# Performance work log

Measured on AMD Instinct MI355X. Metric: run time of the kernel, lower is better.

The kernel has to match this reference:

```python
import jax, jax.numpy as jnp
import numpy as np

N = 50000      # nodes
E = 800000     # edges
IN = 128       # in_dim
OUT = 128      # out_dim
R = 4          # num_relations
H = 8          # heads
D = OUT // H   # per-head dim
NEG_SLOPE = 0.2


def setup_inputs() -> dict:
    key = jax.random.key(0)
    ks = jax.random.split(key, 12)
    s = 0.05
    return {
        "node_inp": jax.random.normal(ks[0], (N, IN), dtype=jnp.float32),
        "edge_index": jax.random.randint(ks[1], (2, E), 0, N),
        "edge_type": jax.random.randint(ks[2], (E,), 0, R),
        # per-relation GATConv params
        "W_rel": jax.random.normal(ks[3], (R, IN, OUT), dtype=jnp.float32) * s,
        "att_src_rel": jax.random.normal(ks[4], (R, H, D), dtype=jnp.float32) * s,
        "att_dst_rel": jax.random.normal(ks[5], (R, H, D), dtype=jnp.float32) * s,
        "bias_rel": jax.random.normal(ks[6], (R, OUT), dtype=jnp.float32) * s,
        # linear layers
        "W_self": jax.random.normal(ks[7], (IN, OUT), dtype=jnp.float32) * s,   # lin_self
        "W_cross": jax.random.normal(ks[8], (OUT, OUT), dtype=jnp.float32) * s,  # lin_cross
        # lang_conv GAT params (lin_l is Bypass, so no weight matrix)
        "att_src_lang": jax.random.normal(ks[9], (H, D), dtype=jnp.float32) * s,
        "att_dst_lang": jax.random.normal(ks[10], (H, D), dtype=jnp.float32) * s,
        "bias_lang": jax.random.normal(ks[11], (OUT,), dtype=jnp.float32) * s,
    }


def _hgnn_forward(node_inp, edge_index, edge_type, W_rel, att_src_rel,
                  att_dst_rel, bias_rel, W_self, W_cross,
                  att_src_lang, att_dst_lang, bias_lang):
    src, dst = edge_index[0], edge_index[1]

    def rel_gat(W, a_s, a_d, b, mask):
        # standard PyG GATConv (single x, add_self_loops=False), restricted to
        # edges with this relation type via mask
        x = (node_inp @ W).reshape(N, H, D)                     # [N,H,D]
        es = jnp.einsum('nhd,hd->nh', x, a_s)
        ed = jnp.einsum('nhd,hd->nh', x, a_d)
        logit = jax.nn.leaky_relu(es[src] + ed[dst], NEG_SLOPE)  # [E,H]
        logit = jnp.where(mask[:, None], logit, -1e30)
        mx = jax.ops.segment_max(logit, dst, num_segments=N)     # [N,H]
        mx = jnp.maximum(mx, -1e30)                              # avoid -inf
        p = jnp.exp(logit - mx[dst]) * mask[:, None]
        den = jax.ops.segment_sum(p, dst, num_segments=N)        # [N,H]
        alpha = p / jnp.where(den > 0, den, 1.0)[dst]            # [E,H]
        msg = alpha[..., None] * x[src]                          # [E,H,D]
        out = jax.ops.segment_sum(msg, dst, num_segments=N)      # [N,H,D]
        tmask = jax.ops.segment_sum(mask.astype(jnp.float32), dst,
                                    num_segments=N) > 0          # [N] target nodes
        return out.reshape(N, OUT) + b, tmask

    rel_masks = edge_type[None, :] == jnp.arange(R)[:, None]     # [R,E]
    rel_out, tmask = jax.vmap(rel_gat)(W_rel, att_src_rel, att_dst_rel,
                                       bias_rel, rel_masks)      # [R,N,OUT],[R,N]
    h = jax.nn.gelu(rel_out, approximate=False) @ W_cross        # [R,N,OUT]

    S = node_inp @ W_self                                        # [N,OUT] self entries
    # lang_conv: per node i, GAT attention over entries {self(i)} U
    # {rel outputs at i for relations where i is a target}. lin_l = Bypass,
    # and since x is a single tensor in PyG, x_dst = rel_inputs[i] = S[i].
    ent = jnp.concatenate([S[None], h], axis=0).reshape(R + 1, N, H, D)
    valid = jnp.concatenate([jnp.ones((1, N), bool), tmask], axis=0)  # [R+1,N]
    ls = jnp.einsum('knhd,hd->knh', ent, att_src_lang)
    ld = jnp.einsum('nhd,hd->nh', ent[0], att_dst_lang)
    logit = jax.nn.leaky_relu(ls + ld[None], NEG_SLOPE)          # [R+1,N,H]
    logit = jnp.where(valid[..., None], logit, -jnp.inf)
    alpha = jax.nn.softmax(logit, axis=0)                        # self always valid
    out = jnp.einsum('knh,knhd->nhd', alpha, ent).reshape(N, OUT)
    return out + bias_lang


def reference(node_inp, edge_index, edge_type, W_rel, att_src_rel, att_dst_rel,
              bias_rel, W_self, W_cross, att_src_lang, att_dst_lang, bias_lang):
    return _hgnn_forward(node_inp, edge_index, edge_type, W_rel, att_src_rel,
                         att_dst_rel, bias_rel, W_self, W_cross,
                         att_src_lang, att_dst_lang, bias_lang)
```

## Files before the change

### kernel.cpp

```cpp
#include <hip/hip_runtime.h>
#include <hip/hip_bf16.h>
#include <math.h>

#define NN 50000
#define NE 800000
#define NREL 4
#define NHEAD 8
#define NSEG (NREL * NN)
#define BCAP 26

typedef __hip_bfloat16 bf16;
typedef short short8 __attribute__((ext_vector_type(8)));
typedef float floatx4 __attribute__((ext_vector_type(4)));

#define LOG2E 1.4426950408889634f

__device__ __forceinline__ float b2f(bf16 v) { return __bfloat162float(v); }
__device__ __forceinline__ float us2f(unsigned short u) {
    return __uint_as_float(((unsigned)u) << 16);
}
__device__ __forceinline__ unsigned short f2us(float v) {
    bf16 b = __float2bfloat16(v);
    return *(unsigned short*)&b;
}

__device__ __forceinline__ float gelu_f(float v) {
    float z = v * 0.70710678118654752f;
    float az = fabsf(z);
    float t = __builtin_amdgcn_rcpf(__builtin_fmaf(0.3275911f, az, 1.f));
    float p = t * (0.254829592f +
              t * (-0.284496736f +
              t * (1.421413741f +
              t * (-1.453152027f +
              t * 1.061405429f))));
    float ex = __builtin_amdgcn_exp2f(az * az * -LOG2E);
    float er = copysignf(1.f - p * ex, z);
    return 0.5f * v * (1.f + er);
}

__global__ void fill_kernel(float* __restrict__ out, int n) {
    int t = blockIdx.x * blockDim.x + threadIdx.x;
    if (t < n) out[t] = 1000.0f;
}

__global__ void prep_kernel(const float* __restrict__ W_rel,
                            const float* __restrict__ W_self,
                            const float* __restrict__ W_cross,
                            const float* __restrict__ a_src,
                            const float* __restrict__ a_dst,
                            bf16* __restrict__ Wt, bf16* __restrict__ Wct,
                            int* __restrict__ counts) {
    int t = blockIdx.x * blockDim.x + threadIdx.x;
    if (t < NSEG) counts[t] = 0;
    if (t < 768 * 128) {
        int row = t >> 7, k = t & 127;
        float v;
        if (row < 512) {
            int r = row >> 7, c = row & 127;
            v = W_rel[(r * 128 + k) * 128 + c];
        } else if (row < 640) {
            v = W_self[k * 128 + (row - 512)];
        } else if (row < 704) {
            int q = row - 640;
            bool is_src = q < 32;
            int qq = is_src ? q : q - 32;
            int r = qq >> 3, h = qq & 7;
            const float* av = (is_src ? a_src : a_dst) + (r * 8 + h) * 16;
            const float* wr = W_rel + (size_t)(r * 128 + k) * 128 + h * 16;
            float s = 0.f;
            #pragma unroll
            for (int dd = 0; dd < 16; ++dd) s += wr[dd] * av[dd];
            v = s * LOG2E;
        } else {
            v = 0.f;
        }
        Wt[t] = __float2bfloat16(v);
    } else if (t < 768 * 128 + 128 * 128) {
        int u = t - 768 * 128;
        int n = u >> 7, k = u & 127;
        Wct[u] = __float2bfloat16(W_cross[k * 128 + n]);
    }
}

__global__ __launch_bounds__(256) void gemm_node(
    const float* __restrict__ Ain,
    const bf16* __restrict__ Bt,
    bf16* __restrict__ outb,
    float* __restrict__ outf,
    unsigned short* __restrict__ es_u,
    unsigned short* __restrict__ ed_u,
    const int* __restrict__ ei,
    const int* __restrict__ et,
    int* __restrict__ counts,
    unsigned short* __restrict__ bkt,
    int M)
{
    if (blockIdx.y == 0) {
        int idx = blockIdx.x * 256 + threadIdx.x;
        int stride = gridDim.x * 256;
        for (int e = idx; e < NE; e += stride) {
            int seg = et[e] * NN + ei[NE + e];
            int pos = atomicAdd(&counts[seg], 1);
            if (pos < BCAP) bkt[(unsigned)seg * BCAP + pos] = (unsigned short)ei[e];
        }
        return;
    }

    __shared__ __align__(16) char smem[17408];
    short (*As)[40] = (short (*)[40])smem;
    short (*Bs)[40] = (short (*)[40])(smem + 5120);

    const int tid  = threadIdx.x;
    const int wave = tid >> 6, lane = tid & 63;
    const int quad = lane >> 4, l16 = lane & 15;
    const int wr_ = wave & 1, wc = wave >> 1;
    const int row0 = blockIdx.x * 64;
    const int col0 = (blockIdx.y - 1) * 128;

    floatx4 acc[2][4];
    #pragma unroll
    for (int i = 0; i < 2; ++i)
        #pragma unroll
        for (int j = 0; j < 4; ++j) acc[i][j] = (floatx4){0.f, 0.f, 0.f, 0.f};

    for (int k0 = 0; k0 < 128; k0 += 32) {
        {
            int c = tid;
            int r = c >> 2, off = (c & 3) * 8;
            int gr = row0 + r;
            short8 v = {0, 0, 0, 0, 0, 0, 0, 0};
            if (gr < M) {
                const float* ap = Ain + (((size_t)gr) << 7) + k0 + off;
                float4 f0 = *(const float4*)ap;
                float4 f1 = *(const float4*)(ap + 4);
                v = (short8){(short)f2us(f0.x), (short)f2us(f0.y),
                             (short)f2us(f0.z), (short)f2us(f0.w),
                             (short)f2us(f1.x), (short)f2us(f1.y),
                             (short)f2us(f1.z), (short)f2us(f1.w)};
            }
            *(short8*)&As[r][off] = v;
        }
        #pragma unroll
        for (int i = 0; i < 2; ++i) {
            int c = tid * 2 + i;
            int r = c >> 2, off = (c & 3) * 8;
            short8 w = *(const short8*)(Bt + (((size_t)(col0 + r)) << 7) + k0 + off);
            *(short8*)&Bs[r][off] = w;
        }
        __syncthreads();

        short8 av[2], bv[4];
        #pragma unroll
        for (int mt = 0; mt < 2; ++mt)
            av[mt] = *(const short8*)&As[wr_ * 32 + mt * 16 + l16][quad * 8];
        #pragma unroll
        for (int nt = 0; nt < 4; ++nt)
            bv[nt] = *(const short8*)&Bs[wc * 64 + nt * 16 + l16][quad * 8];
        #pragma unroll
        for (int mt = 0; mt < 2; ++mt)
            #pragma unroll
            for (int nt = 0; nt < 4; ++nt)
                acc[mt][nt] = __builtin_amdgcn_mfma_f32_16x16x32_bf16(
                    av[mt], bv[nt], acc[mt][nt], 0, 0, 0);
        __syncthreads();
    }

    if (blockIdx.y == 6) {
        if (wc == 0) {
            #pragma unroll
            for (int mt = 0; mt < 2; ++mt) {
                #pragma unroll
                for (int reg = 0; reg < 4; ++reg) {
                    int gr = row0 + wr_ * 32 + mt * 16 + quad * 4 + reg;
                    if (gr >= M) continue;
                    #pragma unroll
                    for (int nt = 0; nt < 4; ++nt) {
                        int q = nt * 16 + l16;
                        unsigned short v = f2us(acc[mt][nt][reg]);
                        if (q < 32)
                            es_u[(unsigned)((q >> 3) * NN + gr) * 8u + (unsigned)(q & 7)] = v;
                        else
                            ed_u[(unsigned)(((q - 32) >> 3) * NN + gr) * 8u + (unsigned)((q - 32) & 7)] = v;
                    }
                }
            }
        }
        return;
    }

    float* ct = (float*)(smem + wave * 4352);
    const int rr2 = lane >> 2;
    const int cc0 = (lane & 3) * 16;

    for (int mt = 0; mt < 2; ++mt) {
        #pragma unroll
        for (int nt = 0; nt < 4; ++nt)
            #pragma unroll
            for (int reg = 0; reg < 4; ++reg)
                ct[(quad * 4 + reg) * 68 + nt * 16 + l16] = acc[mt][nt][reg];
        __syncthreads();

        int gr2 = row0 + wr_ * 32 + mt * 16 + rr2;
        if (gr2 < M) {
            float4 f0 = *(const float4*)&ct[rr2 * 68 + cc0];
            float4 f1 = *(const float4*)&ct[rr2 * 68 + cc0 + 4];
            float4 f2 = *(const float4*)&ct[rr2 * 68 + cc0 + 8];
            float4 f3 = *(const float4*)&ct[rr2 * 68 + cc0 + 12];
            int cb = wc * 64 + cc0;
            if (blockIdx.y == 5) {
                float* dst = outf + (((size_t)gr2) << 7) + cb;
                ((float4*)dst)[0] = f0;
                ((float4*)dst)[1] = f1;
                ((float4*)dst)[2] = f2;
                ((float4*)dst)[3] = f3;
            } else {
                float tmp[16] = {f0.x, f0.y, f0.z, f0.w, f1.x, f1.y, f1.z, f1.w,
                                 f2.x, f2.y, f2.z, f2.w, f3.x, f3.y, f3.z, f3.w};
                short8 o0, o1;
                #pragma unroll
                for (int j = 0; j < 8; ++j) o0[j] = (short)f2us(tmp[j]);
                #pragma unroll
                for (int j = 0; j < 8; ++j) o1[j] = (short)f2us(tmp[8 + j]);
                bf16* dst = outb + ((size_t)((blockIdx.y - 1) * NN + gr2) << 7) + cb;
                *(short8*)dst = o0;
                *(short8*)(dst + 8) = o1;
            }
        }
        __syncthreads();
    }
}

__global__ __launch_bounds__(256) void agg_kernel(
    const unsigned short* __restrict__ bkt, const int* __restrict__ counts,
    const bf16* __restrict__ Xb, const unsigned short* __restrict__ es_u,
    const unsigned short* __restrict__ ed_u, const float* __restrict__ bias_rel,
    bf16* __restrict__ Gb4, unsigned char* __restrict__ flag)
{
    const int rel = blockIdx.y;
    const int n = blockIdx.x * 4 + (threadIdx.x >> 6);
    if (n >= NN) return;
    const int l = threadIdx.x & 63;
    const int h = l >> 3;
    const int f = l * 2;
    const unsigned seg = (unsigned)(rel * NN + n);
    int cnt = __builtin_amdgcn_readfirstlane(counts[seg]);
    cnt = cnt < BCAP ? cnt : BCAP;
    const unsigned short* bk = bkt + seg * (unsigned)BCAP;
    const float edv = us2f(ed_u[seg * 8u + (unsigned)h]);
    float a0 = 0.f, a1 = 0.f, den = 0.f;
    const unsigned short* Xr = (const unsigned short*)Xb + (unsigned)rel * (unsigned)(NN * 128);
    const unsigned short* esr = es_u + (unsigned)rel * (unsigned)(NN * 8);

    int e = 0;
    for (; e + 3 < cnt; e += 4) {
        int s0 = __builtin_amdgcn_readfirstlane((int)bk[e]);
        int s1 = __builtin_amdgcn_readfirstlane((int)bk[e + 1]);
        int s2 = __builtin_amdgcn_readfirstlane((int)bk[e + 2]);
        int s3 = __builtin_amdgcn_readfirstlane((int)bk[e + 3]);
        float e0 = us2f(esr[(unsigned)s0 * 8u + (unsigned)h]);
        float e1 = us2f(esr[(unsigned)s1 * 8u + (unsigned)h]);
        float e2 = us2f(esr[(unsigned)s2 * 8u + (unsigned)h]);
        float e3 = us2f(esr[(unsigned)s3 * 8u + (unsigned)h]);
        ushort2 u0 = *(const ushort2*)(Xr + (unsigned)s0 * 128u + (unsigned)f);
        ushort2 u1 = *(const ushort2*)(Xr + (unsigned)s1 * 128u + (unsigned)f);
        ushort2 u2 = *(const ushort2*)(Xr + (unsigned)s2 * 128u + (unsigned)f);
        ushort2 u3 = *(const ushort2*)(Xr + (unsigned)s3 * 128u + (unsigned)f);
        float aa0 = e0 + edv, aa1 = e1 + edv, aa2 = e2 + edv, aa3 = e3 + edv;
        float w0 = __builtin_amdgcn_exp2f(fmaxf(aa0, 0.2f * aa0));
        float w1 = __builtin_amdgcn_exp2f(fmaxf(aa1, 0.2f * aa1));
        float w2 = __builtin_amdgcn_exp2f(fmaxf(aa2, 0.2f * aa2));
        float w3 = __builtin_amdgcn_exp2f(fmaxf(aa3, 0.2f * aa3));
        a0 += w0 * us2f(u0.x) + w1 * us2f(u1.x) + w2 * us2f(u2.x) + w3 * us2f(u3.x);
        a1 += w0 * us2f(u0.y) + w1 * us2f(u1.y) + w2 * us2f(u2.y) + w3 * us2f(u3.y);
        den += (w0 + w1) + (w2 + w3);
    }
    for (; e < cnt; ++e) {
        int s0 = __builtin_amdgcn_readfirstlane((int)bk[e]);
        float e0 = us2f(esr[(unsigned)s0 * 8u + (unsigned)h]);
        ushort2 u0 = *(const ushort2*)(Xr + (unsigned)s0 * 128u + (unsigned)f);
        float aa0 = e0 + edv;
        float w0 = __builtin_amdgcn_exp2f(fmaxf(aa0, 0.2f * aa0));
        a0 += w0 * us2f(u0.x);
        a1 += w0 * us2f(u0.y);
        den += w0;
    }

    float inv = den > 0.f ? __builtin_amdgcn_rcpf(den) : 0.f;
    float2 bv = *(const float2*)(bias_rel + (unsigned)rel * 128u + (unsigned)f);
    float v0 = gelu_f(__builtin_fmaf(a0, inv, bv.x));
    float v1 = gelu_f(__builtin_fmaf(a1, inv, bv.y));
    ushort2 o;
    o.x = f2us(v0);
    o.y = f2us(v1);
    *(ushort2*)((unsigned short*)Gb4 + ((unsigned)n * 4u + (unsigned)rel) * 128u + (unsigned)f) = o;
    if (l == 0) flag[(unsigned)n * 4u + (unsigned)rel] = (unsigned char)(cnt > 0);
}

__global__ __launch_bounds__(256) void gemm_lang(
    const bf16* __restrict__ A,
    const bf16* __restrict__ Bt,
    const unsigned char* __restrict__ flag,
    const float* __restrict__ asl_g,
    const float* __restrict__ adl_g,
    const float* __restrict__ bias_lang,
    float* __restrict__ out)
{
    __shared__ __align__(16) char smem[15360];
    short (*As)[40] = (short (*)[40])smem;
    short (*Bs)[40] = (short (*)[40])(smem + 5120);

    const int M = NN * NREL;
    const int tid  = threadIdx.x;
    const int wave = tid >> 6, lane = tid & 63;
    const int quad = lane >> 4, l16 = lane & 15;
    const int wr_ = wave & 1, wc = wave >> 1;
    const int row0 = blockIdx.x * 64;

    floatx4 acc[2][4];
    #pragma unroll
    for (int i = 0; i < 2; ++i)
        #pragma unroll
        for (int j = 0; j < 4; ++j) acc[i][j] = (floatx4){0.f, 0.f, 0.f, 0.f};

    for (int k0 = 0; k0 < 128; k0 += 32) {
        {
            int c = tid;
            int r = c >> 2, off = (c & 3) * 8;
            int gr = row0 + r;
            short8 v = {0, 0, 0, 0, 0, 0, 0, 0};
            if (gr < M)
                v = *(const short8*)(A + (((size_t)gr) << 7) + k0 + off);
            *(short8*)&As[r][off] = v;
        }
        #pragma unroll
        for (int i = 0; i < 2; ++i) {
            int c = tid * 2 + i;
            int r = c >> 2, off = (c & 3) * 8;
            short8 w = *(const short8*)(Bt + (((size_t)r) << 7) + k0 + off);
            *(short8*)&Bs[r][off] = w;
        }
        __syncthreads();

        short8 av[2], bv[4];
        #pragma unroll
        for (int mt = 0; mt < 2; ++mt)
            av[mt] = *(const short8*)&As[wr_ * 32 + mt * 16 + l16][quad * 8];
        #pragma unroll
        for (int nt = 0; nt < 4; ++nt)
            bv[nt] = *(const short8*)&Bs[wc * 64 + nt * 16 + l16][quad * 8];
        #pragma unroll
        for (int mt = 0; mt < 2; ++mt)
            #pragma unroll
            for (int nt = 0; nt < 4; ++nt)
                acc[mt][nt] = __builtin_amdgcn_mfma_f32_16x16x32_bf16(
                    av[mt], bv[nt], acc[mt][nt], 0, 0, 0);
        __syncthreads();
    }

    const int nb0 = blockIdx.x * 16 + wr_ * 8;
    #pragma unroll
    for (int nt = 0; nt < 4; ++nt) {
        int col = wc * 64 + nt * 16 + l16;
        float asl = asl_g[col];
        float adl = adl_g[col];
        float bl  = bias_lang[col];
        #pragma unroll
        for (int mt = 0; mt < 2; ++mt) {
            int node = nb0 + mt * 4 + quad;
            bool ok = node < NN;
            float Sv = ok ? out[(unsigned)node * 128u + (unsigned)col] : 0.f;
            float h0 = acc[mt][nt][0], h1 = acc[mt][nt][1];
            float h2 = acc[mt][nt][2], h3 = acc[mt][nt][3];
            float t0 = h0 * asl, t1 = h1 * asl, t2 = h2 * asl, t3 = h3 * asl;
            float ts = Sv * asl, td = Sv * adl;
            #pragma unroll
            for (int off = 1; off < 16; off <<= 1) {
                t0 += __shfl_xor(t0, off);
                t1 += __shfl_xor(t1, off);
                t2 += __shfl_xor(t2, off);
                t3 += __shfl_xor(t3, off);
                ts += __shfl_xor(ts, off);
                td += __shfl_xor(td, off);
            }
            unsigned fl = ok ? *(const unsigned*)(flag + (unsigned)node * 4u) : 0u;
            float aS = ts + td, a0 = t0 + td, a1 = t1 + td, a2 = t2 + td, a3 = t3 + td;
            float lS = fmaxf(aS, 0.2f * aS);
            float l0 = fmaxf(a0, 0.2f * a0);
            float l1 = fmaxf(a1, 0.2f * a1);
            float l2 = fmaxf(a2, 0.2f * a2);
            float l3 = fmaxf(a3, 0.2f * a3);
            bool v0 = (fl & 0x000000FFu) != 0, v1 = (fl & 0x0000FF00u) != 0;
            bool v2 = (fl & 0x00FF0000u) != 0, v3 = (fl & 0xFF000000u) != 0;
            float m = lS;
            if (v0) m = fmaxf(m, l0);
            if (v1) m = fmaxf(m, l1);
            if (v2) m = fmaxf(m, l2);
            if (v3) m = fmaxf(m, l3);
            float eS = __expf(lS - m);
            float e0 = v0 ? __expf(l0 - m) : 0.f;
            float e1 = v1 ? __expf(l1 - m) : 0.f;
            float e2 = v2 ? __expf(l2 - m) : 0.f;
            float e3 = v3 ? __expf(l3 - m) : 0.f;
            float sum = eS + e0 + e1 + e2 + e3;
            float o = eS * Sv + e0 * h0 + e1 * h1 + e2 * h2 + e3 * h3;
            o = o / sum + bl;
            if (ok) out[(unsigned)node * 128u + (unsigned)col] = o;
        }
    }
}

extern "C" void kernel_launch(void* const* d_in, const int* in_sizes, int n_in,
                              void* d_out, int out_size, void* d_ws, size_t ws_size,
                              hipStream_t stream) {
    const float* node_inp     = (const float*)d_in[0];
    const int*   edge_index   = (const int*)d_in[1];
    const int*   edge_type    = (const int*)d_in[2];
    const float* W_rel        = (const float*)d_in[3];
    const float* att_src_rel  = (const float*)d_in[4];
    const float* att_dst_rel  = (const float*)d_in[5];
    const float* bias_rel     = (const float*)d_in[6];
    const float* W_self       = (const float*)d_in[7];
    const float* W_cross      = (const float*)d_in[8];
    const float* att_src_lang = (const float*)d_in[9];
    const float* att_dst_lang = (const float*)d_in[10];
    const float* bias_lang    = (const float*)d_in[11];
    (void)in_sizes; (void)n_in;

    const size_t SZ_XB   = (size_t)NREL * NN * 128 * 2;
    const size_t SZ_ES   = (size_t)NREL * NN * 8 * 2;
    const size_t SZ_GB4  = (size_t)NREL * NN * 128 * 2;
    const size_t SZ_WT   = 768 * 128 * 2;
    const size_t SZ_WCT  = 128 * 128 * 2;
    const size_t SZ_BKT  = (size_t)NSEG * BCAP * 2;
    const size_t SZ_CNT  = (size_t)NSEG * 4;
    const size_t SZ_FLG  = (size_t)NN * 4;
    const size_t TOTAL = SZ_XB + 2 * SZ_ES + SZ_GB4 + SZ_WT + SZ_WCT +
                         SZ_BKT + SZ_CNT + SZ_FLG;

    if (ws_size < TOTAL) {
        fill_kernel<<<(out_size + 255) / 256, 256, 0, stream>>>((float*)d_out, out_size);
        return;
    }

    char* ws = (char*)d_ws;
    size_t o = 0;
    bf16*  Xb      = (bf16*)(ws + o);  o += SZ_XB;
    unsigned short* es_u = (unsigned short*)(ws + o); o += SZ_ES;
    unsigned short* ed_u = (unsigned short*)(ws + o); o += SZ_ES;
    bf16*  Gb4     = (bf16*)(ws + o);  o += SZ_GB4;
    bf16*  Wt      = (bf16*)(ws + o);  o += SZ_WT;
    bf16*  Wct     = (bf16*)(ws + o);  o += SZ_WCT;
    unsigned short* bkt = (unsigned short*)(ws + o); o += SZ_BKT;
    int*   counts  = (int*)(ws + o);   o += SZ_CNT;
    unsigned char* flag = (unsigned char*)(ws + o);
    float* S       = (float*)d_out;

    prep_kernel<<<(NSEG + 255) / 256, 256, 0, stream>>>(
        W_rel, W_self, W_cross, att_src_rel, att_dst_rel, Wt, Wct, counts);

    dim3 g1((NN + 63) / 64, 7);
    gemm_node<<<g1, 256, 0, stream>>>(node_inp, Wt, Xb, S, es_u, ed_u,
                                      edge_index, edge_type, counts, bkt, NN);

    dim3 ga((NN + 3) / 4, NREL);
    agg_kernel<<<ga, 256, 0, stream>>>(bkt, counts, Xb, es_u, ed_u, bias_rel, Gb4, flag);

    dim3 g2((NREL * NN + 63) / 64, 1);
    gemm_lang<<<g2, 256, 0, stream>>>(Gb4, Wct, flag, att_src_lang, att_dst_lang,
                                      bias_lang, (float*)d_out);
}
```

Before: 297.4 us.

## Load A tile once per block and loop over all six column tiles

The node GEMM previously launched one block per 128-column output tile, so each of the six column tiles re-read and re-converted the fp32 input rows. Now each block converts its 64-row A tile to bf16 once, holds it in registers, and loops over the six column tiles, reading B fragments directly from global memory and dropping the B shared-memory staging. Per-wave block syncs in the epilogue are replaced by a waitcnt because each wave uses a private staging area. The grid shrinks from 7 to 2 in y, which cuts parallelism and serializes more work per block, and there is more register pressure from the held A fragments.

```diff
diff --git a/kernel.cpp b/kernel.cpp
--- a/kernel.cpp
+++ b/kernel.cpp
@@ -106,127 +106,127 @@
         return;
     }
 
-    __shared__ __align__(16) char smem[17408];
-    short (*As)[40] = (short (*)[40])smem;
-    short (*Bs)[40] = (short (*)[40])(smem + 5120);
+    __shared__ __align__(16) char smem[20480];
+    short (*As)[64][40] = (short (*)[64][40])smem;
 
     const int tid  = threadIdx.x;
     const int wave = tid >> 6, lane = tid & 63;
     const int quad = lane >> 4, l16 = lane & 15;
     const int wr_ = wave & 1, wc = wave >> 1;
     const int row0 = blockIdx.x * 64;
-    const int col0 = (blockIdx.y - 1) * 128;
-
-    floatx4 acc[2][4];
-    #pragma unroll
-    for (int i = 0; i < 2; ++i)
-        #pragma unroll
-        for (int j = 0; j < 4; ++j) acc[i][j] = (floatx4){0.f, 0.f, 0.f, 0.f};
-
-    for (int k0 = 0; k0 < 128; k0 += 32) {
-        {
-            int c = tid;
-            int r = c >> 2, off = (c & 3) * 8;
-            int gr = row0 + r;
+
+    {
+        int r = tid >> 2, kc = tid & 3;
+        int gr = row0 + r;
+        const float* ap = Ain + (((size_t)gr) << 7) + kc * 32;
+        #pragma unroll
+        for (int i = 0; i < 4; ++i) {
             short8 v = {0, 0, 0, 0, 0, 0, 0, 0};
             if (gr < M) {
-                const float* ap = Ain + (((size_t)gr) << 7) + k0 + off;
-                float4 f0 = *(const float4*)ap;
-                float4 f1 = *(const float4*)(ap + 4);
+                float4 f0 = *(const float4*)(ap + i * 8);
+                float4 f1 = *(const float4*)(ap + i * 8 + 4);
                 v = (short8){(short)f2us(f0.x), (short)f2us(f0.y),
                              (short)f2us(f0.z), (short)f2us(f0.w),
                              (short)f2us(f1.x), (short)f2us(f1.y),
                              (short)f2us(f1.z), (short)f2us(f1.w)};
             }
-            *(short8*)&As[r][off] = v;
-        }
-        #pragma unroll
-        for (int i = 0; i < 2; ++i) {
-            int c = tid * 2 + i;
-            int r = c >> 2, off = (c & 3) * 8;
-            short8 w = *(const short8*)(Bt + (((size_t)(col0 + r)) << 7) + k0 + off);
-            *(short8*)&Bs[r][off] = w;
-        }
-        __syncthreads();
-
-        short8 av[2], bv[4];
+            *(short8*)&As[kc][r][i * 8] = v;
+        }
+    }
+    __syncthreads();
+
+    short8 av[4][2];
+    #pragma unroll
+    for (int kc = 0; kc < 4; ++kc)
         #pragma unroll
         for (int mt = 0; mt < 2; ++mt)
-            av[mt] = *(const short8*)&As[wr_ * 32 + mt * 16 + l16][quad * 8];
-        #pragma unroll
-        for (int nt = 0; nt < 4; ++nt)
-            bv[nt] = *(const short8*)&Bs[wc * 64 + nt * 16 + l16][quad * 8];
-        #pragma unroll
-        for (int mt = 0; mt < 2; ++mt)
+            av[kc][mt] = *(const short8*)&As[kc][wr_ * 32 + mt * 16 + l16][quad * 8];
+    __syncthreads();
+
+    float* ct = (float*)(smem + wave * 4352);
+    const int rr2 = lane >> 2;
+    const int cc0 = (lane & 3) * 16;
+
+    #pragma unroll 1
+    for (int t = 0; t < 6; ++t) {
+        floatx4 acc[2][4];
+        #pragma unroll
+        for (int i = 0; i < 2; ++i)
+            #pragma unroll
+            for (int j = 0; j < 4; ++j) acc[i][j] = (floatx4){0.f, 0.f, 0.f, 0.f};
+
+        #pragma unroll
+        for (int kc = 0; kc < 4; ++kc) {
+            short8 bv[4];
             #pragma unroll
             for (int nt = 0; nt < 4; ++nt)
-                acc[mt][nt] = __builtin_amdgcn_mfma_f32_16x16x32_bf16(
-                    av[mt], bv[nt], acc[mt][nt], 0, 0, 0);
-        __syncthreads();
-    }
-
-    if (blockIdx.y == 6) {
-        if (wc == 0) {
-            #pragma unroll
-            for (int mt = 0; mt < 2; ++mt) {
+                bv[nt] = *(const short8*)(Bt +
+                    (((size_t)(t * 128 + wc * 64 + nt * 16 + l16)) << 7) + kc * 32 + quad * 8);
+            #pragma unroll
+            for (int mt = 0; mt < 2; ++mt)
                 #pragma unroll
-                for (int reg = 0; reg < 4; ++reg) {
-                    int gr = row0 + wr_ * 32 + mt * 16 + quad * 4 + reg;
-                    if (gr >= M) continue;
+                for (int nt = 0; nt < 4; ++nt)
+                    acc[mt][nt] = __builtin_amdgcn_mfma_f32_16x16x32_bf16(
+                        av[kc][mt], bv[nt], acc[mt][nt], 0, 0, 0);
+        }
+
+        if (t == 5) {
+            if (wc == 0) {
+                #pragma unroll
+                for (int mt = 0; mt < 2; ++mt) {
                     #pragma unroll
-                    for (int nt = 0; nt < 4; ++nt) {
-                        int q = nt * 16 + l16;
-                        unsigned short v = f2us(acc[mt][nt][reg]);
-                        if (q < 32)
-                            es_u[(unsigned)((q >> 3) * NN + gr) * 8u + (unsigned)(q & 7)] = v;
-                        else
-                            ed_u[(unsigned)(((q - 32) >> 3) * NN + gr) * 8u + (unsigned)((q - 32) & 7)] = v;
+                    for (int reg = 0; reg < 4; ++reg) {
+                        int gr = row0 + wr_ * 32 + mt * 16 + quad * 4 + reg;
+                        if (gr >= M) continue;
+                        #pragma unroll
+                        for (int nt = 0; nt < 4; ++nt) {
+                            int q = nt * 16 + l16;
+                            unsigned short v = f2us(acc[mt][nt][reg]);
+                            if (q < 32)
+                                es_u[(unsigned)((q >> 3) * NN + gr) * 8u + (unsigned)(q & 7)] = v;
+                            else
+                                ed_u[(unsigned)(((q - 32) >> 3) * NN + gr) * 8u + (unsigned)((q - 32) & 7)] = v;
+                        }
                     }
                 }
             }
-        }
-        return;
-    }
-
-    float* ct = (float*)(smem + wave * 4352);
-    const int rr2 = lane >> 2;
-    const int cc0 = (lane & 3) * 16;
-
-    for (int mt = 0; mt < 2; ++mt) {
-        #pragma unroll
-        for (int nt = 0; nt < 4; ++nt)
-            #pragma unroll
-            for (int reg = 0; reg < 4; ++reg)
-                ct[(quad * 4 + reg) * 68 + nt * 16 + l16] = acc[mt][nt][reg];
-        __syncthreads();
-
-        int gr2 = row0 + wr_ * 32 + mt * 16 + rr2;
-        if (gr2 < M) {
-            float4 f0 = *(const float4*)&ct[rr2 * 68 + cc0];
-            float4 f1 = *(const float4*)&ct[rr2 * 68 + cc0 + 4];
-            float4 f2 = *(const float4*)&ct[rr2 * 68 + cc0 + 8];
-            float4 f3 = *(const float4*)&ct[rr2 * 68 + cc0 + 12];
-            int cb = wc * 64 + cc0;
-            if (blockIdx.y == 5) {
-                float* dst = outf + (((size_t)gr2) << 7) + cb;
-                ((float4*)dst)[0] = f0;
-                ((float4*)dst)[1] = f1;
-                ((float4*)dst)[2] = f2;
-                ((float4*)dst)[3] = f3;
-            } else {
-                float tmp[16] = {f0.x, f0.y, f0.z, f0.w, f1.x, f1.y, f1.z, f1.w,
-                                 f2.x, f2.y, f2.z, f2.w, f3.x, f3.y, f3.z, f3.w};
-                short8 o0, o1;
+        } else {
+            for (int mt = 0; mt < 2; ++mt) {
                 #pragma unroll
-                for (int j = 0; j < 8; ++j) o0[j] = (short)f2us(tmp[j]);
-                #pragma unroll
-                for (int j = 0; j < 8; ++j) o1[j] = (short)f2us(tmp[8 + j]);
-                bf16* dst = outb + ((size_t)((blockIdx.y - 1) * NN + gr2) << 7) + cb;
-                *(short8*)dst = o0;
-                *(short8*)(dst + 8) = o1;
+                for (int nt = 0; nt < 4; ++nt)
+                    #pragma unroll
+                    for (int reg = 0; reg < 4; ++reg)
+                        ct[(quad * 4 + reg) * 68 + nt * 16 + l16] = acc[mt][nt][reg];
+                __builtin_amdgcn_s_waitcnt(0);
+
+                int gr2 = row0 + wr_ * 32 + mt * 16 + rr2;
+                if (gr2 < M) {
+                    float4 f0 = *(const float4*)&ct[rr2 * 68 + cc0];
+                    float4 f1 = *(const float4*)&ct[rr2 * 68 + cc0 + 4];
+                    float4 f2 = *(const float4*)&ct[rr2 * 68 + cc0 + 8];
+                    float4 f3 = *(const float4*)&ct[rr2 * 68 + cc0 + 12];
+                    int cb = wc * 64 + cc0;
+                    if (t == 4) {
+                        float* dst = outf + (((size_t)gr2) << 7) + cb;
+                        ((float4*)dst)[0] = f0;
+                        ((float4*)dst)[1] = f1;
+                        ((float4*)dst)[2] = f2;
+                        ((float4*)dst)[3] = f3;
+                    } else {
+                        float tmp[16] = {f0.x, f0.y, f0.z, f0.w, f1.x, f1.y, f1.z, f1.w,
+                                         f2.x, f2.y, f2.z, f2.w, f3.x, f3.y, f3.z, f3.w};
+                        short8 o0, o1;
+                        #pragma unroll
+                        for (int j = 0; j < 8; ++j) o0[j] = (short)f2us(tmp[j]);
+                        #pragma unroll
+                        for (int j = 0; j < 8; ++j) o1[j] = (short)f2us(tmp[8 + j]);
+                        bf16* dst = outb + ((size_t)(t * NN + gr2) << 7) + cb;
+                        *(short8*)dst = o0;
+                        *(short8*)(dst + 8) = o1;
+                    }
+                }
             }
         }
-        __syncthreads();
     }
 }
 
@@ -458,7 +458,7 @@
     prep_kernel<<<(NSEG + 255) / 256, 256, 0, stream>>>(
         W_rel, W_self, W_cross, att_src_rel, att_dst_rel, Wt, Wct, counts);
 
-    dim3 g1((NN + 63) / 64, 7);
+    dim3 g1((NN + 63) / 64, 2);
     gemm_node<<<g1, 256, 0, stream>>>(node_inp, Wt, Xb, S, es_u, ed_u,
                                       edge_index, edge_type, counts, bkt, NN);
 
```

After: 322.2 us. 8.3% more time.
